# Optimization experiments

Measured on AMD Instinct MI355X. Metric: run time of the kernel, lower is better.

Reference implementation:

```python
import jax, jax.numpy as jnp
import numpy as np

B, L, D, H, NL, C = 8, 512, 64, 256, 2, 8
EPS = 1e-5
NEG = -1e9


def _causal_softmax(scores):
    # scores: (B, L, L); lower-triangular causal mask then softmax over last dim
    Ls = scores.shape[-1]
    mask = jnp.tril(jnp.ones((Ls, Ls), dtype=bool))
    return jax.nn.softmax(jnp.where(mask, scores, NEG), axis=-1)


def _attn_plain(x):
    s = jnp.einsum('bld,bmd->blm', x, x)
    return jnp.einsum('blm,bmd->bld', _causal_softmax(s), x)


def _attn_sdpa(x):
    s = jnp.einsum('bld,bmd->blm', x, x) / jnp.sqrt(jnp.float32(x.shape[-1]))
    return jnp.einsum('blm,bmd->bld', _causal_softmax(s), x)


def _attn_additive(x):
    # materializes (B, L, L, D) as in the original module
    s = jnp.tanh(x[:, :, None, :] + x[:, None, :, :]).sum(axis=-1)  # (B,L,L)
    return jnp.einsum('blm,bmd->bld', _causal_softmax(s), x)


def _bn(x, gamma, beta):
    # training-mode BatchNorm1d over (B, L) per feature; x: (B, L, F)
    mu = x.mean(axis=(0, 1))
    var = ((x - mu) ** 2).mean(axis=(0, 1))
    return (x - mu) * jax.lax.rsqrt(var + EPS) * gamma + beta


def _lstm_layer(x, Wih, Whh, bih, bhh):
    # x: (B, L, K) -> (B, L, H). PyTorch gate order: i, f, g, o.
    Hh = Whh.shape[1]
    xg = jnp.einsum('blk,gk->blg', x, Wih) + bih + bhh  # (B, L, 4H)
    xg = jnp.swapaxes(xg, 0, 1)  # (L, B, 4H)

    def step(carry, xt):
        h, c = carry
        g = xt + h @ Whh.T
        i = jax.nn.sigmoid(g[:, 0 * Hh:1 * Hh])
        f = jax.nn.sigmoid(g[:, 1 * Hh:2 * Hh])
        gg = jnp.tanh(g[:, 2 * Hh:3 * Hh])
        o = jax.nn.sigmoid(g[:, 3 * Hh:4 * Hh])
        c = f * c + i * gg
        h = o * jnp.tanh(c)
        return (h, c), h

    h0 = jnp.zeros((x.shape[0], Hh), x.dtype)
    _, hs = jax.lax.scan(step, (h0, h0), xg)
    return jnp.swapaxes(hs, 0, 1)  # (B, L, H)


def setup_inputs() -> dict:
    key = jax.random.key(0)
    ks = jax.random.split(key, 20)
    s = 1.0 / np.sqrt(H)
    u = lambda k, sh: jax.random.uniform(k, sh, jnp.float32, -s, s)
    return {
        'src': jax.random.normal(ks[0], (B, L, D), jnp.float32),
        'attn_w': jax.random.uniform(ks[1], (3, L, D), jnp.float32, 0.5, 1.5),
        'cat_w': jax.random.uniform(ks[2], (3, L, H), jnp.float32, 0.5, 1.5),
        'bn1_gamma': 1.0 + 0.1 * jax.random.normal(ks[3], (3, D), jnp.float32),
        'bn1_beta': 0.1 * jax.random.normal(ks[4], (3, D), jnp.float32),
        'bn2_gamma': 1.0 + 0.1 * jax.random.normal(ks[5], (H,), jnp.float32),
        'bn2_beta': 0.1 * jax.random.normal(ks[6], (H,), jnp.float32),
        'Wih0': u(ks[7], (3, 4 * H, D)),
        'Whh0': u(ks[8], (3, 4 * H, H)),
        'bih0': u(ks[9], (3, 4 * H)),
        'bhh0': u(ks[10], (3, 4 * H)),
        'Wih1': u(ks[11], (3, 4 * H, H)),
        'Whh1': u(ks[12], (3, 4 * H, H)),
        'bih1': u(ks[13], (3, 4 * H)),
        'bhh1': u(ks[14], (3, 4 * H)),
        'fc_W': u(ks[15], (C, H)),
        'fc_b': u(ks[16], (C,)),
    }


def reference(src, attn_w, cat_w, bn1_gamma, bn1_beta, bn2_gamma, bn2_beta,
              Wih0, Whh0, bih0, bhh0, Wih1, Whh1, bih1, bhh1, fc_W, fc_b):
    # three attentions, normalized weighted sum
    outs = jnp.stack([_attn_plain(src), _attn_additive(src), _attn_sdpa(src)])  # (3,B,L,D)
    aw = attn_w / attn_w.sum(axis=0)  # (3, L, D)
    attention_output = jnp.einsum('kbld,kld->bld', outs, aw)

    line1 = _bn(src, bn1_gamma[0], bn1_beta[0])
    line2 = _bn(src + attention_output, bn1_gamma[1], bn1_beta[1])
    line3 = _bn(attention_output, bn1_gamma[2], bn1_beta[2])

    def lstm2(x, i):
        h = _lstm_layer(x, Wih0[i], Whh0[i], bih0[i], bhh0[i])
        return _lstm_layer(h, Wih1[i], Whh1[i], bih1[i], bhh1[i])

    l1 = lstm2(line1, 0)
    l2 = lstm2(line2, 1)
    l3 = lstm2(line3, 2)

    cw = cat_w / cat_w.sum(axis=0)  # (3, L, H)
    cat = l1 * cw[0] + l2 * cw[1] + l3 * cw[2]
    cat = _bn(cat, bn2_gamma, bn2_beta)
    # eval-mode dropout is identity
    return cat[:, -1, :] @ fc_W.T + fc_b  # (B, C)
```

## Files before the change

### kernel.cpp

```cpp
#include <hip/hip_runtime.h>

#define B_ 8
#define L_ 512
#define D_ 64
#define H_ 256
#define GH 1024
#define EPS_ 1e-5f
#define POISON_ 0xAAAAAAAAu

typedef float f32x4 __attribute__((ext_vector_type(4)));
typedef _Float16 half8 __attribute__((ext_vector_type(8)));

__device__ __forceinline__ unsigned short f2h(float f) {
  _Float16 h = (_Float16)f;
  return __builtin_bit_cast(unsigned short, h);
}
__device__ __forceinline__ float h2f(unsigned short s) {
  _Float16 h = __builtin_bit_cast(_Float16, s);
  return (float)h;
}
__device__ __forceinline__ float fast_tanh(float x) {
  return 1.0f - 2.0f / (1.0f + __expf(2.0f * x));
}
__device__ __forceinline__ float fast_sig(float x) {
  return 1.0f / (1.0f + __expf(-x));
}
__device__ __forceinline__ unsigned int load_agent(const unsigned int* p) {
  return __hip_atomic_load(p, __ATOMIC_RELAXED, __HIP_MEMORY_SCOPE_AGENT);
}

__global__ void scores_kernel(const float* __restrict__ src,
                              float* __restrict__ Sp, float* __restrict__ Sa) {
  const int l = blockIdx.x, b = blockIdx.y;
  __shared__ float xl[D_];
  if (threadIdx.x < D_) xl[threadIdx.x] = src[(b * L_ + l) * D_ + threadIdx.x];
  __syncthreads();
  for (int m = threadIdx.x; m <= l; m += blockDim.x) {
    const float4* xr = (const float4*)&src[(b * L_ + m) * D_];
    float dp = 0.f, da = 0.f;
#pragma unroll
    for (int d4 = 0; d4 < D_ / 4; ++d4) {
      float4 v = xr[d4];
      dp += xl[d4*4+0]*v.x + xl[d4*4+1]*v.y + xl[d4*4+2]*v.z + xl[d4*4+3]*v.w;
      da += fast_tanh(xl[d4*4+0]+v.x) + fast_tanh(xl[d4*4+1]+v.y)
          + fast_tanh(xl[d4*4+2]+v.z) + fast_tanh(xl[d4*4+3]+v.w);
    }
    Sp[(b * L_ + l) * L_ + m] = dp;
    Sa[(b * L_ + l) * L_ + m] = da;
  }
}

__global__ void softmax_av_kernel(const float* __restrict__ src, const float* __restrict__ Sp,
                                  const float* __restrict__ Sa, float* __restrict__ outk) {
  const int l = blockIdx.x, b = blockIdx.y, k = blockIdx.z;
  const int lane = threadIdx.x;
  __shared__ float p[L_];
  const float* row = (k == 1) ? &Sa[(b * L_ + l) * L_] : &Sp[(b * L_ + l) * L_];
  const float scale = (k == 2) ? 0.125f : 1.0f;
  float mx = -1e30f;
  for (int m = lane; m <= l; m += 64) { float v = row[m] * scale; p[m] = v; mx = fmaxf(mx, v); }
#pragma unroll
  for (int off = 32; off > 0; off >>= 1) mx = fmaxf(mx, __shfl_xor(mx, off, 64));
  float sum = 0.f;
  for (int m = lane; m <= l; m += 64) { float e = __expf(p[m] - mx); p[m] = e; sum += e; }
#pragma unroll
  for (int off = 32; off > 0; off >>= 1) sum += __shfl_xor(sum, off, 64);
  __syncthreads();
  const float inv = 1.0f / sum;
  float acc = 0.f;
  for (int m = 0; m <= l; ++m) acc += p[m] * src[(b * L_ + m) * D_ + lane];
  outk[((k * B_ + b) * L_ + l) * D_ + lane] = acc * inv;
}

__global__ void combine_kernel(const float* __restrict__ outk, const float* __restrict__ attn_w,
                               float* __restrict__ attn) {
  int i = blockIdx.x * blockDim.x + threadIdx.x;
  if (i >= B_ * L_ * D_) return;
  int ld = i & (L_ * D_ - 1);
  float w0 = attn_w[ld], w1 = attn_w[L_ * D_ + ld], w2 = attn_w[2 * L_ * D_ + ld];
  float o0 = outk[i], o1 = outk[B_ * L_ * D_ + i], o2 = outk[2 * B_ * L_ * D_ + i];
  attn[i] = (o0 * w0 + o1 * w1 + o2 * w2) / (w0 + w1 + w2);
}

__global__ void bn1_kernel(const float* __restrict__ src, const float* __restrict__ attn,
                           const float* __restrict__ gamma, const float* __restrict__ beta,
                           float* __restrict__ line_in) {
  const int d = blockIdx.x, line = blockIdx.y;
  float s1 = 0.f, s2 = 0.f;
  for (int i = threadIdx.x; i < B_ * L_; i += blockDim.x) {
    float v = (line == 0) ? src[i * D_ + d]
            : (line == 1) ? src[i * D_ + d] + attn[i * D_ + d]
                          : attn[i * D_ + d];
    s1 += v; s2 += v * v;
  }
#pragma unroll
  for (int off = 32; off > 0; off >>= 1) { s1 += __shfl_xor(s1, off, 64); s2 += __shfl_xor(s2, off, 64); }
  __shared__ float a1[4], a2[4];
  __shared__ float mean_s, rstd_s;
  int w = threadIdx.x >> 6;
  if ((threadIdx.x & 63) == 0) { a1[w] = s1; a2[w] = s2; }
  __syncthreads();
  if (threadIdx.x == 0) {
    float t1 = a1[0] + a1[1] + a1[2] + a1[3];
    float t2 = a2[0] + a2[1] + a2[2] + a2[3];
    float mean = t1 / (float)(B_ * L_);
    float var = t2 / (float)(B_ * L_) - mean * mean;
    mean_s = mean; rstd_s = rsqrtf(var + EPS_);
  }
  __syncthreads();
  const float mean = mean_s;
  const float gs = gamma[line * D_ + d] * rstd_s, be = beta[line * D_ + d];
  for (int i = threadIdx.x; i < B_ * L_; i += blockDim.x) {
    float v = (line == 0) ? src[i * D_ + d]
            : (line == 1) ? src[i * D_ + d] + attn[i * D_ + d]
                          : attn[i * D_ + d];
    line_in[line * B_ * L_ * D_ + i * D_ + d] = (v - mean) * gs + be;
  }
}

template <int IN_K>
__device__ __forceinline__ void rec_body(
    const float* __restrict__ in_f32,
    const unsigned short* __restrict__ in_b16,
    const float* __restrict__ Wih, const float* __restrict__ Whh,
    const float* __restrict__ bih, const float* __restrict__ bhh,
    unsigned short* __restrict__ hseq,
    int line, int s,
    unsigned short* hprev, unsigned short* inbuf,
    float (*gbuf)[32][8], float (*biasS)[32]) {
  constexpr int INROW = IN_K + 8;
  constexpr int NKT_IN = IN_K / 32;
  const int tid = threadIdx.x, w = tid >> 6, lane = tid & 63;
  const int q = lane >> 4, col = lane & 15;

  half8 whhF[2][8];
  half8 wihF[2][NKT_IN];
#pragma unroll
  for (int T = 0; T < 2; ++T) {
    const int n = w * H_ + s * 32 + T * 16 + col;
    const float* wr = &Whh[(line * GH + n) * H_];
#pragma unroll
    for (int kt = 0; kt < 8; ++kt) {
      const float* pk = wr + kt * 32 + q * 8;
      half8 t;
#pragma unroll
      for (int j = 0; j < 8; ++j) t[j] = (_Float16)pk[j];
      whhF[T][kt] = t;
    }
    const float* wr2 = &Wih[(line * GH + n) * IN_K];
#pragma unroll
    for (int kt = 0; kt < NKT_IN; ++kt) {
      const float* pk = wr2 + kt * 32 + q * 8;
      half8 t;
#pragma unroll
      for (int j = 0; j < 8; ++j) t[j] = (_Float16)pk[j];
      wihF[T][kt] = t;
    }
  }
  if (tid < 128) {
    int g = tid >> 5, j = tid & 31;
    int n = g * H_ + s * 32 + j;
    biasS[g][j] = bih[line * GH + n] + bhh[line * GH + n];
  }
  for (int i = tid; i < 16 * 264; i += 256) hprev[i] = 0;
  for (int i = tid; i < 16 * INROW; i += 256) inbuf[i] = 0;

  int gdst[4];
  bool gremote[4];
  int goff[4];
#pragma unroll
  for (int rr = 0; rr < 4; ++rr) {
    int u = tid + rr * 256;
    int r = u >> 7, v = u & 127, b = v >> 4, pz = v & 15;
    int cidx = r * 32 + pz * 2;
    gremote[rr] = (r != s);
    gdst[rr] = b * 264 + cidx;
    goff[rr] = b * H_ + cidx;
  }

  if constexpr (IN_K == 64) {
#pragma unroll
    for (int r = 0; r < 2; ++r) {
      int idx = tid + r * 256;
      int b = idx >> 6, d = idx & 63;
      inbuf[b * INROW + d] = f2h(in_f32[(line * B_ * L_ + b * L_ + 0) * D_ + d]);
    }
  } else {
    const unsigned int* sa[4];
    unsigned int sv[4];
#pragma unroll
    for (int r = 0; r < 4; ++r) {
      int u = tid + r * 256;
      int b = u >> 7, pr = u & 127;
      sa[r] = (const unsigned int*)&in_b16[((line * L_ + 0) * B_ + b) * H_ + pr * 2];
    }
    bool ready = false;
    while (!ready) {
#pragma unroll
      for (int r = 0; r < 4; ++r) sv[r] = load_agent(sa[r]);
      ready = true;
#pragma unroll
      for (int r = 0; r < 4; ++r) ready = ready && (sv[r] != POISON_);
    }
#pragma unroll
    for (int r = 0; r < 4; ++r) {
      int u = tid + r * 256;
      int b = u >> 7, pr = u & 127;
      *(unsigned int*)&inbuf[b * INROW + pr * 2] = sv[r];
    }
  }

  float c0 = 0.f, c1 = 0.f;
  const int ub = tid & 7, jp = (tid >> 3) * 2;
  __syncthreads();

  for (int t = 0; t < L_; ++t) {
    f32x4 acc0 = {0.f, 0.f, 0.f, 0.f}, acc1 = {0.f, 0.f, 0.f, 0.f};
#pragma unroll
    for (int kt = 0; kt < NKT_IN; ++kt) {
      half8 a = *(const half8*)&inbuf[col * INROW + kt * 32 + q * 8];
      acc0 = __builtin_amdgcn_mfma_f32_16x16x32_f16(a, wihF[0][kt], acc0, 0, 0, 0);
      acc1 = __builtin_amdgcn_mfma_f32_16x16x32_f16(a, wihF[1][kt], acc1, 0, 0, 0);
    }
#pragma unroll
    for (int kt = 0; kt < 8; ++kt) {
      half8 a = *(const half8*)&hprev[col * 264 + kt * 32 + q * 8];
      acc0 = __builtin_amdgcn_mfma_f32_16x16x32_f16(a, whhF[0][kt], acc0, 0, 0, 0);
      acc1 = __builtin_amdgcn_mfma_f32_16x16x32_f16(a, whhF[1][kt], acc1, 0, 0, 0);
    }
    if (q < 2) {
#pragma unroll
      for (int r = 0; r < 4; ++r) {
        gbuf[w][col][q * 4 + r] = acc0[r];
        gbuf[w][16 + col][q * 4 + r] = acc1[r];
      }
    }
    __syncthreads();

    if (tid < 128) {
      float gi0 = gbuf[0][jp][ub] + biasS[0][jp];
      float gf0 = gbuf[1][jp][ub] + biasS[1][jp];
      float gg0 = gbuf[2][jp][ub] + biasS[2][jp];
      float go0 = gbuf[3][jp][ub] + biasS[3][jp];
      float gi1 = gbuf[0][jp+1][ub] + biasS[0][jp+1];
      float gf1 = gbuf[1][jp+1][ub] + biasS[1][jp+1];
      float gg1 = gbuf[2][jp+1][ub] + biasS[2][jp+1];
      float go1 = gbuf[3][jp+1][ub] + biasS[3][jp+1];
      c0 = fast_sig(gf0) * c0 + fast_sig(gi0) * fast_tanh(gg0);
      c1 = fast_sig(gf1) * c1 + fast_sig(gi1) * fast_tanh(gg1);
      float h0 = fast_sig(go0) * fast_tanh(c0);
      float h1 = fast_sig(go1) * fast_tanh(c1);
      unsigned int packed = (unsigned int)f2h(h0) | ((unsigned int)f2h(h1) << 16);
      if (packed == POISON_) packed ^= 1u;
      __hip_atomic_store(
          (unsigned int*)&hseq[((line * L_ + t) * B_ + ub) * H_ + s * 32 + jp],
          packed, __ATOMIC_RELAXED, __HIP_MEMORY_SCOPE_AGENT);
      *(unsigned int*)&hprev[ub * 264 + s * 32 + jp] = packed;
    }

    if (t == L_ - 1) break;

    const unsigned short* hrow = &hseq[(size_t)(line * L_ + t) * B_ * H_];
    const unsigned int* ga[4];
    unsigned int gv[4];
#pragma unroll
    for (int rr = 0; rr < 4; ++rr) ga[rr] = (const unsigned int*)(hrow + goff[rr]);

    if constexpr (IN_K == 64) {
#pragma unroll
      for (int r = 0; r < 2; ++r) {
        int idx = tid + r * 256;
        int b = idx >> 6, d = idx & 63;
        inbuf[b * INROW + d] = f2h(in_f32[(line * B_ * L_ + b * L_ + t + 1) * D_ + d]);
      }
      bool ready = false;
      while (!ready) {
#pragma unroll
        for (int rr = 0; rr < 4; ++rr) gv[rr] = load_agent(ga[rr]);
        ready = true;
#pragma unroll
        for (int rr = 0; rr < 4; ++rr)
          ready = ready && (!gremote[rr] || gv[rr] != POISON_);
      }
    } else {
      const unsigned int* sa[4];
      unsigned int sv[4];
#pragma unroll
      for (int r = 0; r < 4; ++r) {
        int u = tid + r * 256;
        int b = u >> 7, pr = u & 127;
        sa[r] = (const unsigned int*)&in_b16[((line * L_ + t + 1) * B_ + b) * H_ + pr * 2];
      }
      bool ready = false;
      while (!ready) {
#pragma unroll
        for (int rr = 0; rr < 4; ++rr) gv[rr] = load_agent(ga[rr]);
#pragma unroll
        for (int r = 0; r < 4; ++r) sv[r] = load_agent(sa[r]);
        ready = true;
#pragma unroll
        for (int rr = 0; rr < 4; ++rr)
          ready = ready && (!gremote[rr] || gv[rr] != POISON_);
#pragma unroll
        for (int r = 0; r < 4; ++r) ready = ready && (sv[r] != POISON_);
      }
#pragma unroll
      for (int r = 0; r < 4; ++r) {
        int u = tid + r * 256;
        int b = u >> 7, pr = u & 127;
        *(unsigned int*)&inbuf[b * INROW + pr * 2] = sv[r];
      }
    }
#pragma unroll
    for (int rr = 0; rr < 4; ++rr)
      if (gremote[rr]) *(unsigned int*)&hprev[gdst[rr]] = gv[rr];
    __syncthreads();
  }
}

__global__ __launch_bounds__(256, 1) void rec_fused_kernel(
    const float* __restrict__ line_in,
    const float* __restrict__ Wih0, const float* __restrict__ Whh0,
    const float* __restrict__ bih0, const float* __restrict__ bhh0,
    const float* __restrict__ Wih1, const float* __restrict__ Whh1,
    const float* __restrict__ bih1, const float* __restrict__ bhh1,
    unsigned short* __restrict__ hseq0, unsigned short* __restrict__ hseq1) {
  __shared__ unsigned short hprev[16 * 264];
  __shared__ unsigned short inbuf[16 * 264];
  __shared__ float gbuf[4][32][8];
  __shared__ float biasS[4][32];
  const int blk = blockIdx.x;
  const int layer = blk / 24, rem = blk % 24;
  const int line = rem >> 3, s = rem & 7;
  if (layer == 0)
    rec_body<64>(line_in, nullptr, Wih0, Whh0, bih0, bhh0, hseq0,
                 line, s, hprev, inbuf, gbuf, biasS);
  else
    rec_body<256>(nullptr, hseq0, Wih1, Whh1, bih1, bhh1, hseq1,
                  line, s, hprev, inbuf, gbuf, biasS);
}

__global__ void bn2stats_kernel(const unsigned short* __restrict__ hseq1,
                                const float* __restrict__ cat_w, float* __restrict__ stats) {
  const int h = blockIdx.x;
  float s1 = 0.f, s2 = 0.f;
  for (int i = threadIdx.x; i < B_ * L_; i += blockDim.x) {
    int l = i >> 3, b = i & 7;
    float w0 = cat_w[(0 * L_ + l) * H_ + h], w1 = cat_w[(1 * L_ + l) * H_ + h],
          w2 = cat_w[(2 * L_ + l) * H_ + h];
    float v0 = h2f(hseq1[((0 * L_ + l) * B_ + b) * H_ + h]);
    float v1 = h2f(hseq1[((1 * L_ + l) * B_ + b) * H_ + h]);
    float v2 = h2f(hseq1[((2 * L_ + l) * B_ + b) * H_ + h]);
    float v = (v0 * w0 + v1 * w1 + v2 * w2) / (w0 + w1 + w2);
    s1 += v; s2 += v * v;
  }
#pragma unroll
  for (int off = 32; off > 0; off >>= 1) { s1 += __shfl_xor(s1, off, 64); s2 += __shfl_xor(s2, off, 64); }
  __shared__ float a1[4], a2[4];
  int w = threadIdx.x >> 6;
  if ((threadIdx.x & 63) == 0) { a1[w] = s1; a2[w] = s2; }
  __syncthreads();
  if (threadIdx.x == 0) {
    float t1 = a1[0] + a1[1] + a1[2] + a1[3];
    float t2 = a2[0] + a2[1] + a2[2] + a2[3];
    float mean = t1 / (float)(B_ * L_);
    float var = t2 / (float)(B_ * L_) - mean * mean;
    stats[2 * h] = mean;
    stats[2 * h + 1] = rsqrtf(var + EPS_);
  }
}

__global__ void final_kernel(const unsigned short* __restrict__ hseq1,
                             const float* __restrict__ cat_w, const float* __restrict__ stats,
                             const float* __restrict__ gamma, const float* __restrict__ beta,
                             const float* __restrict__ fcW, const float* __restrict__ fcb,
                             float* __restrict__ out) {
  const int h = threadIdx.x;
  __shared__ float vmat[B_][H_];
  const float mean = stats[2 * h], rstd = stats[2 * h + 1];
  const float g = gamma[h], be = beta[h];
  const int l = L_ - 1;
  float w0 = cat_w[(0 * L_ + l) * H_ + h], w1 = cat_w[(1 * L_ + l) * H_ + h],
        w2 = cat_w[(2 * L_ + l) * H_ + h];
  const float wsum = w0 + w1 + w2;
  for (int b = 0; b < B_; ++b) {
    float v0 = h2f(hseq1[((0 * L_ + l) * B_ + b) * H_ + h]);
    float v1 = h2f(hseq1[((1 * L_ + l) * B_ + b) * H_ + h]);
    float v2 = h2f(hseq1[((2 * L_ + l) * B_ + b) * H_ + h]);
    float v = (v0 * w0 + v1 * w1 + v2 * w2) / wsum;
    vmat[b][h] = (v - mean) * rstd * g + be;
  }
  __syncthreads();
  if (h < 64) {
    int b = h >> 3, c = h & 7;
    float acc = fcb[c];
    for (int k = 0; k < H_; ++k) acc += vmat[b][k] * fcW[c * H_ + k];
    out[b * 8 + c] = acc;
  }
}

extern "C" void kernel_launch(void* const* d_in, const int* in_sizes, int n_in,
                              void* d_out, int out_size, void* d_ws, size_t ws_size,
                              hipStream_t stream) {
  (void)in_sizes; (void)n_in; (void)out_size; (void)ws_size;
  const float* src       = (const float*)d_in[0];
  const float* attn_w    = (const float*)d_in[1];
  const float* cat_w     = (const float*)d_in[2];
  const float* bn1_gamma = (const float*)d_in[3];
  const float* bn1_beta  = (const float*)d_in[4];
  const float* bn2_gamma = (const float*)d_in[5];
  const float* bn2_beta  = (const float*)d_in[6];
  const float* Wih0      = (const float*)d_in[7];
  const float* Whh0      = (const float*)d_in[8];
  const float* bih0      = (const float*)d_in[9];
  const float* bhh0      = (const float*)d_in[10];
  const float* Wih1      = (const float*)d_in[11];
  const float* Whh1      = (const float*)d_in[12];
  const float* bih1      = (const float*)d_in[13];
  const float* bhh1      = (const float*)d_in[14];
  const float* fcW       = (const float*)d_in[15];
  const float* fcb       = (const float*)d_in[16];
  float* out = (float*)d_out;

  char* p = (char*)d_ws;
  float* Sp = (float*)p;                      p += (size_t)B_ * L_ * L_ * 4;
  float* Sa = (float*)p;                      p += (size_t)B_ * L_ * L_ * 4;
  float* outk = (float*)p;                    p += (size_t)3 * B_ * L_ * D_ * 4;
  float* attn = (float*)p;                    p += (size_t)B_ * L_ * D_ * 4;
  float* line_in = (float*)p;                 p += (size_t)3 * B_ * L_ * D_ * 4;
  float* stats = (float*)p;                   p += (size_t)512 * 4;
  unsigned short* hseq0 = (unsigned short*)p; p += (size_t)3 * L_ * B_ * H_ * 2;
  unsigned short* hseq1 = (unsigned short*)p; p += (size_t)3 * L_ * B_ * H_ * 2;

  scores_kernel<<<dim3(L_, B_), dim3(256), 0, stream>>>(src, Sp, Sa);
  softmax_av_kernel<<<dim3(L_, B_, 3), dim3(64), 0, stream>>>(src, Sp, Sa, outk);
  combine_kernel<<<dim3((B_ * L_ * D_) / 256), dim3(256), 0, stream>>>(outk, attn_w, attn);
  bn1_kernel<<<dim3(D_, 3), dim3(256), 0, stream>>>(src, attn, bn1_gamma, bn1_beta, line_in);
  rec_fused_kernel<<<dim3(48), dim3(256), 0, stream>>>(
      line_in, Wih0, Whh0, bih0, bhh0, Wih1, Whh1, bih1, bhh1, hseq0, hseq1);
  bn2stats_kernel<<<dim3(H_), dim3(256), 0, stream>>>(hseq1, cat_w, stats);
  final_kernel<<<dim3(1), dim3(256), 0, stream>>>(hseq1, cat_w, stats, bn2_gamma, bn2_beta,
                                                  fcW, fcb, out);
}
```

Before: 1.300 ms.

## Fuse attention scores and softmax-AV kernels; add s_sleep backoff to spin waits

Merges the score and softmax/AV kernels into one kernel that keeps each score row in shared memory. This removes the 16 MB global round trip for the Sp/Sa matrices and one launch, with three wavefronts handling the three attention variants. It also adds s_sleep backoff to the inter-block polling loops in the recurrent kernel, which cuts memory traffic from spinning but may add wake-up latency on the critical serial path. The fused attention kernel leaves its fourth wave idle during the softmax/AV phase and runs fewer blocks in parallel for that phase.

```diff
diff --git a/kernel.cpp b/kernel.cpp
--- a/kernel.cpp
+++ b/kernel.cpp
@@ -29,13 +29,15 @@
   return __hip_atomic_load(p, __ATOMIC_RELAXED, __HIP_MEMORY_SCOPE_AGENT);
 }
 
-__global__ void scores_kernel(const float* __restrict__ src,
-                              float* __restrict__ Sp, float* __restrict__ Sa) {
+__global__ void attn_kernel(const float* __restrict__ src, float* __restrict__ outk) {
   const int l = blockIdx.x, b = blockIdx.y;
+  const int tid = threadIdx.x, w = tid >> 6, lane = tid & 63;
   __shared__ float xl[D_];
-  if (threadIdx.x < D_) xl[threadIdx.x] = src[(b * L_ + l) * D_ + threadIdx.x];
-  __syncthreads();
-  for (int m = threadIdx.x; m <= l; m += blockDim.x) {
+  __shared__ float sp[L_], sa[L_];
+  __shared__ float pk[3][L_];
+  if (tid < D_) xl[tid] = src[(b * L_ + l) * D_ + tid];
+  __syncthreads();
+  for (int m = tid; m <= l; m += 256) {
     const float4* xr = (const float4*)&src[(b * L_ + m) * D_];
     float dp = 0.f, da = 0.f;
 #pragma unroll
@@ -45,31 +47,33 @@
       da += fast_tanh(xl[d4*4+0]+v.x) + fast_tanh(xl[d4*4+1]+v.y)
           + fast_tanh(xl[d4*4+2]+v.z) + fast_tanh(xl[d4*4+3]+v.w);
     }
-    Sp[(b * L_ + l) * L_ + m] = dp;
-    Sa[(b * L_ + l) * L_ + m] = da;
-  }
-}
-
-__global__ void softmax_av_kernel(const float* __restrict__ src, const float* __restrict__ Sp,
-                                  const float* __restrict__ Sa, float* __restrict__ outk) {
-  const int l = blockIdx.x, b = blockIdx.y, k = blockIdx.z;
-  const int lane = threadIdx.x;
-  __shared__ float p[L_];
-  const float* row = (k == 1) ? &Sa[(b * L_ + l) * L_] : &Sp[(b * L_ + l) * L_];
-  const float scale = (k == 2) ? 0.125f : 1.0f;
-  float mx = -1e30f;
-  for (int m = lane; m <= l; m += 64) { float v = row[m] * scale; p[m] = v; mx = fmaxf(mx, v); }
-#pragma unroll
-  for (int off = 32; off > 0; off >>= 1) mx = fmaxf(mx, __shfl_xor(mx, off, 64));
-  float sum = 0.f;
-  for (int m = lane; m <= l; m += 64) { float e = __expf(p[m] - mx); p[m] = e; sum += e; }
-#pragma unroll
-  for (int off = 32; off > 0; off >>= 1) sum += __shfl_xor(sum, off, 64);
-  __syncthreads();
-  const float inv = 1.0f / sum;
-  float acc = 0.f;
-  for (int m = 0; m <= l; ++m) acc += p[m] * src[(b * L_ + m) * D_ + lane];
-  outk[((k * B_ + b) * L_ + l) * D_ + lane] = acc * inv;
+    sp[m] = dp;
+    sa[m] = da;
+  }
+  __syncthreads();
+  if (w < 3) {
+    const float scale = (w == 2) ? 0.125f : 1.0f;
+    float mx = -1e30f;
+    for (int m = lane; m <= l; m += 64) {
+      float v = ((w == 1) ? sa[m] : sp[m]) * scale;
+      pk[w][m] = v;
+      mx = fmaxf(mx, v);
+    }
+#pragma unroll
+    for (int off = 32; off > 0; off >>= 1) mx = fmaxf(mx, __shfl_xor(mx, off, 64));
+    float sum = 0.f;
+    for (int m = lane; m <= l; m += 64) {
+      float e = __expf(pk[w][m] - mx);
+      pk[w][m] = e;
+      sum += e;
+    }
+#pragma unroll
+    for (int off = 32; off > 0; off >>= 1) sum += __shfl_xor(sum, off, 64);
+    const float inv = 1.0f / sum;
+    float acc = 0.f;
+    for (int m = 0; m <= l; ++m) acc += pk[w][m] * src[(b * L_ + m) * D_ + lane];
+    outk[((w * B_ + b) * L_ + l) * D_ + lane] = acc * inv;
+  }
 }
 
 __global__ void combine_kernel(const float* __restrict__ outk, const float* __restrict__ attn_w,
@@ -194,13 +198,16 @@
       int b = u >> 7, pr = u & 127;
       sa[r] = (const unsigned int*)&in_b16[((line * L_ + 0) * B_ + b) * H_ + pr * 2];
     }
-    bool ready = false;
-    while (!ready) {
+    int miss = 0;
+    for (;;) {
 #pragma unroll
       for (int r = 0; r < 4; ++r) sv[r] = load_agent(sa[r]);
-      ready = true;
+      bool ready = true;
 #pragma unroll
       for (int r = 0; r < 4; ++r) ready = ready && (sv[r] != POISON_);
+      if (ready) break;
+      if (miss == 0) { asm volatile("s_sleep 1"); miss = 1; }
+      else asm volatile("s_sleep 4");
     }
 #pragma unroll
     for (int r = 0; r < 4; ++r) {
@@ -273,14 +280,17 @@
         int b = idx >> 6, d = idx & 63;
         inbuf[b * INROW + d] = f2h(in_f32[(line * B_ * L_ + b * L_ + t + 1) * D_ + d]);
       }
-      bool ready = false;
-      while (!ready) {
+      int miss = 0;
+      for (;;) {
 #pragma unroll
         for (int rr = 0; rr < 4; ++rr) gv[rr] = load_agent(ga[rr]);
-        ready = true;
+        bool ready = true;
 #pragma unroll
         for (int rr = 0; rr < 4; ++rr)
           ready = ready && (!gremote[rr] || gv[rr] != POISON_);
+        if (ready) break;
+        if (miss == 0) { asm volatile("s_sleep 1"); miss = 1; }
+        else asm volatile("s_sleep 4");
       }
     } else {
       const unsigned int* sa[4];
@@ -291,18 +301,21 @@
         int b = u >> 7, pr = u & 127;
         sa[r] = (const unsigned int*)&in_b16[((line * L_ + t + 1) * B_ + b) * H_ + pr * 2];
       }
-      bool ready = false;
-      while (!ready) {
+      int miss = 0;
+      for (;;) {
 #pragma unroll
         for (int rr = 0; rr < 4; ++rr) gv[rr] = load_agent(ga[rr]);
 #pragma unroll
         for (int r = 0; r < 4; ++r) sv[r] = load_agent(sa[r]);
-        ready = true;
+        bool ready = true;
 #pragma unroll
         for (int rr = 0; rr < 4; ++rr)
           ready = ready && (!gremote[rr] || gv[rr] != POISON_);
 #pragma unroll
         for (int r = 0; r < 4; ++r) ready = ready && (sv[r] != POISON_);
+        if (ready) break;
+        if (miss == 0) { asm volatile("s_sleep 1"); miss = 1; }
+        else asm volatile("s_sleep 4");
       }
 #pragma unroll
       for (int r = 0; r < 4; ++r) {
@@ -423,8 +436,6 @@
   float* out = (float*)d_out;
 
   char* p = (char*)d_ws;
-  float* Sp = (float*)p;                      p += (size_t)B_ * L_ * L_ * 4;
-  float* Sa = (float*)p;                      p += (size_t)B_ * L_ * L_ * 4;
   float* outk = (float*)p;                    p += (size_t)3 * B_ * L_ * D_ * 4;
   float* attn = (float*)p;                    p += (size_t)B_ * L_ * D_ * 4;
   float* line_in = (float*)p;                 p += (size_t)3 * B_ * L_ * D_ * 4;
@@ -432,8 +443,7 @@
   unsigned short* hseq0 = (unsigned short*)p; p += (size_t)3 * L_ * B_ * H_ * 2;
   unsigned short* hseq1 = (unsigned short*)p; p += (size_t)3 * L_ * B_ * H_ * 2;
 
-  scores_kernel<<<dim3(L_, B_), dim3(256), 0, stream>>>(src, Sp, Sa);
-  softmax_av_kernel<<<dim3(L_, B_, 3), dim3(64), 0, stream>>>(src, Sp, Sa, outk);
+  attn_kernel<<<dim3(L_, B_), dim3(256), 0, stream>>>(src, outk);
   combine_kernel<<<dim3((B_ * L_ * D_) / 256), dim3(256), 0, stream>>>(outk, attn_w, attn);
   bn1_kernel<<<dim3(D_, 3), dim3(256), 0, stream>>>(src, attn, bn1_gamma, bn1_beta, line_in);
   rec_fused_kernel<<<dim3(48), dim3(256), 0, stream>>>(
```

Measured after the change: 1.307 ms. Within noise of the previous version (+0.5%).
